# Optimization experiments

Hardware: AMD Instinct MI355X
Metric: run time of the kernel (lower is better)

Reference implementation:

```python
import jax, jax.numpy as jnp
import numpy as np

FILTERS = 512
DQK = FILTERS // 8  # 64


def setup_inputs() -> dict:
    key = jax.random.key(0)
    ks = jax.random.split(key, 7)
    B, H, W, C = 32, 32, 32, FILTERS
    x = jax.random.normal(ks[0], (B, H, W, C), dtype=jnp.float32)
    # 1x1 convs == per-pixel dense layers: weight [Cin, Cout], bias [Cout]
    def glorot(k, cin, cout):
        lim = np.sqrt(6.0 / (cin + cout)).astype(np.float32)
        return jax.random.uniform(k, (cin, cout), jnp.float32, -lim, lim)
    return {
        "x": x,
        "wq": glorot(ks[1], C, DQK), "bq": jnp.zeros((DQK,), jnp.float32),
        "wk": glorot(ks[2], C, DQK), "bk": jnp.zeros((DQK,), jnp.float32),
        "wv": glorot(ks[3], C, C),   "bv": jnp.zeros((C,), jnp.float32),
    }


def reference(x, wq, bq, wk, bk, wv, bv):
    B, H, W, C = x.shape
    N = H * W
    xf = x.reshape(B, N, C)                       # flatten spatial -> tokens
    q = xf @ wq + bq                              # [B, N, C//8]
    k = xf @ wk + bk                              # [B, N, C//8]
    v = xf @ wv + bv                              # [B, N, C]
    scale = 1.0 / jnp.sqrt(jnp.float32(C // 8))
    scores = jnp.einsum('bnd,bmd->bnm', q, k) * scale  # [B, N, N]
    probs = jax.nn.softmax(scores, axis=-1)
    attended = jnp.einsum('bnm,bmc->bnc', probs, v)    # [B, N, C]
    return attended.reshape(B, H, W, C) + x
```

## Files before the change

### kernel.cpp

```cpp
#include <hip/hip_runtime.h>
#include <stdint.h>

#define B_ 32
#define N_ 1024
#define C_ 512
#define D_ 64

typedef __attribute__((ext_vector_type(8))) __bf16 bf8;
typedef __attribute__((ext_vector_type(4))) float f32x4;

typedef const __attribute__((address_space(1))) void* gp_t;
typedef __attribute__((address_space(3))) void* lp_t;

__device__ inline void g2l16(const void* g, void* l) {
    __builtin_amdgcn_global_load_lds((gp_t)g, (lp_t)l, 16, 0, 0);
}

__device__ inline float b2f(unsigned short u) {
    return __uint_as_float(((unsigned)u) << 16);
}
__device__ inline unsigned short f2b(float f) {
    unsigned u = __float_as_uint(f);
    u += 0x7FFF + ((u >> 16) & 1);
    return (unsigned short)(u >> 16);
}

#define MFMA16(a, b, c) __builtin_amdgcn_mfma_f32_16x16x32_bf16((a), (b), (c), 0, 0, 0)

__device__ __forceinline__ void ld_frags(const unsigned short* As, const unsigned short* Bs,
                                         int wm, int wn, int lane,
                                         bf8 (&a)[2][4], bf8 (&bb)[2][4]) {
    #pragma unroll
    for (int kq = 0; kq < 2; ++kq) {
        #pragma unroll
        for (int ti = 0; ti < 4; ++ti)
            a[kq][ti] = *(const bf8*)&As[((wm * 4 + ti) * 2 + kq) * 512 + lane * 8];
        #pragma unroll
        for (int tj = 0; tj < 4; ++tj)
            bb[kq][tj] = *(const bf8*)&Bs[((wn * 4 + tj) * 2 + kq) * 512 + lane * 8];
    }
}

__device__ __forceinline__ void do_mfma(const bf8 (&a)[2][4], const bf8 (&bb)[2][4],
                                        f32x4 (&acc)[4][4]) {
    #pragma unroll
    for (int kq = 0; kq < 2; ++kq)
        #pragma unroll
        for (int ti = 0; ti < 4; ++ti)
            #pragma unroll
            for (int tj = 0; tj < 4; ++tj)
                acc[ti][tj] = MFMA16(a[kq][ti], bb[kq][tj], acc[ti][tj]);
}

__global__ __launch_bounds__(256) void prep(
    const float* __restrict__ x, unsigned short* __restrict__ xb,
    const float* __restrict__ wq, const float* __restrict__ wk,
    const float* __restrict__ wv, unsigned short* __restrict__ wt)
{
    int bid = blockIdx.x;
    if (bid < 16384) {
        int i = bid * 256 + threadIdx.x;
        float4 f = ((const float4*)x)[i];
        ushort4 o;
        o.x = f2b(f.x); o.y = f2b(f.y); o.z = f2b(f.z); o.w = f2b(f.w);
        ((ushort4*)xb)[i] = o;
    } else {
        int t = (bid - 16384) * 256 + threadIdx.x;
        int co = t >> 9;
        int ci = t & 511;
        const float* src;
        int col, cout;
        if (co < 64)       { src = wq; col = co;       cout = 64;  }
        else if (co < 128) { src = wk; col = co - 64;  cout = 64;  }
        else               { src = wv; col = co - 128; cout = 512; }
        wt[t] = f2b(src[(size_t)ci * cout + col]);
    }
}

__global__ __launch_bounds__(256) void qkv(
    const unsigned short* __restrict__ xb,
    const unsigned short* __restrict__ WT,
    const float* __restrict__ bq, const float* __restrict__ bk,
    const float* __restrict__ bv,
    unsigned short* __restrict__ q, unsigned short* __restrict__ k,
    unsigned short* __restrict__ vT)
{
    const int f_  = blockIdx.x;
    const int xcd = f_ & 7;
    const int s_  = f_ >> 3;
    const int rb  = xcd * 32 + s_ / 5;
    const int cb  = s_ % 5;

    const int tid = threadIdx.x;
    const int lane = tid & 63;
    const int wave = tid >> 6;
    const int wm = wave >> 1, wn = wave & 1;
    const int lr = lane & 15;
    const int lk = lane >> 4;

    __shared__ unsigned short SM[32768];
    unsigned short* TB = SM;

    const int row0 = rb * 128;
    const int col0 = cb * 128;

    f32x4 zero4 = {0.f, 0.f, 0.f, 0.f};
    f32x4 acc[4][4];
    #pragma unroll
    for (int i = 0; i < 4; ++i)
        #pragma unroll
        for (int j = 0; j < 4; ++j) acc[i][j] = zero4;

    auto stage = [&](int buf, int kk) {
        unsigned short* As = SM + buf * 8192;
        unsigned short* Bs = SM + 16384 + buf * 8192;
        #pragma unroll
        for (int i = 0; i < 4; ++i) {
            int f = wave * 4 + i;
            int t = f >> 1, kq = f & 1;
            g2l16(xb + (size_t)(row0 + t * 16 + lr) * C_ + kk + kq * 32 + lk * 8,
                  &As[f * 512]);
            g2l16(WT + (size_t)(col0 + t * 16 + lr) * C_ + kk + kq * 32 + lk * 8,
                  &Bs[f * 512]);
        }
    };

    stage(0, 0);
    stage(1, 64);
    int cur = 0;
    for (int t = 0; t < 6; ++t) {
        asm volatile("s_waitcnt vmcnt(8)" ::: "memory");
        __builtin_amdgcn_s_barrier();
        bf8 a[2][4], bb[2][4];
        ld_frags(SM + cur * 8192, SM + 16384 + cur * 8192, wm, wn, lane, a, bb);
        asm volatile("s_waitcnt lgkmcnt(0)" ::: "memory");
        __builtin_amdgcn_s_barrier();
        stage(cur, (t + 2) * 64);
        do_mfma(a, bb, acc);
        cur ^= 1;
    }
    {
        asm volatile("s_waitcnt vmcnt(8)" ::: "memory");
        __builtin_amdgcn_s_barrier();
        bf8 a[2][4], bb[2][4];
        ld_frags(SM + cur * 8192, SM + 16384 + cur * 8192, wm, wn, lane, a, bb);
        do_mfma(a, bb, acc);
        cur ^= 1;
    }
    {
        asm volatile("s_waitcnt vmcnt(0)" ::: "memory");
        __builtin_amdgcn_s_barrier();
        bf8 a[2][4], bb[2][4];
        ld_frags(SM + cur * 8192, SM + 16384 + cur * 8192, wm, wn, lane, a, bb);
        do_mfma(a, bb, acc);
    }

    if (cb == 0) {
        unsigned short* outp = (wn == 0) ? q : k;
        const float* bias = (wn == 0) ? bq : bk;
        #pragma unroll
        for (int ti = 0; ti < 4; ++ti)
            #pragma unroll
            for (int tj = 0; tj < 4; ++tj) {
                int col = tj * 16 + lr;
                float bi = bias[col];
                #pragma unroll
                for (int r = 0; r < 4; ++r) {
                    int row = row0 + wm * 64 + ti * 16 + lk * 4 + r;
                    outp[(size_t)row * D_ + col] = f2b(acc[ti][tj][r] + bi);
                }
            }
    } else {
        const int colv = (cb - 1) * 128;
        __syncthreads();
        #pragma unroll
        for (int ti = 0; ti < 4; ++ti)
            #pragma unroll
            for (int tj = 0; tj < 4; ++tj) {
                int c = wn * 64 + tj * 16 + lr;
                float bi = bv[colv + c];
                int tok = wm * 64 + ti * 16 + lk * 4;
                ushort4 o;
                o.x = f2b(acc[ti][tj][0] + bi);
                o.y = f2b(acc[ti][tj][1] + bi);
                o.z = f2b(acc[ti][tj][2] + bi);
                o.w = f2b(acc[ti][tj][3] + bi);
                *(ushort4*)&TB[c * 132 + tok] = o;
            }
        __syncthreads();
        const int b  = row0 >> 10;
        const int n0 = row0 & 1023;
        #pragma unroll
        for (int i = 0; i < 16; ++i) {
            int idx = tid + 256 * i;
            int c = idx >> 5, ch = idx & 31;
            ushort4 t4 = *(const ushort4*)&TB[c * 132 + ch * 4];
            *(ushort4*)&vT[((size_t)(b * C_ + colv + c)) * N_ + n0 + ch * 4] = t4;
        }
    }
}

#define SLD 1032
__global__ __launch_bounds__(256) void scores(
    const unsigned short* __restrict__ q,
    const unsigned short* __restrict__ k,
    unsigned short* __restrict__ P)
{
    const int f_  = blockIdx.x;
    const int xcd = f_ & 7;
    const int s_  = f_ >> 3;
    const int b   = xcd * 4 + (s_ >> 6);
    const int qt  = s_ & 63;

    const int tid = threadIdx.x, lane = tid & 63, wave = tid >> 6;
    const int lr = lane & 15, lk = lane >> 4;
    __shared__ unsigned short S[16 * SLD];

    const int n0 = qt * 16;
    const unsigned short* qrow = q + (size_t)(b * N_ + n0 + lr) * D_ + lk * 8;
    bf8 qa0 = *(const bf8*)(qrow);
    bf8 qa1 = *(const bf8*)(qrow + 32);

    const int m0w = wave * 256;
    #pragma unroll 4
    for (int mt = 0; mt < 16; ++mt) {
        int m = m0w + mt * 16;
        const unsigned short* krow = k + (size_t)(b * N_ + m + lr) * D_ + lk * 8;
        bf8 kb0 = *(const bf8*)(krow);
        bf8 kb1 = *(const bf8*)(krow + 32);
        f32x4 s = {0.f, 0.f, 0.f, 0.f};
        s = MFMA16(qa0, kb0, s);
        s = MFMA16(qa1, kb1, s);
        #pragma unroll
        for (int r = 0; r < 4; ++r)
            S[(lk * 4 + r) * SLD + m + lr] = f2b(s[r] * 0.125f);
    }
    __syncthreads();

    #pragma unroll
    for (int rr4 = 0; rr4 < 4; ++rr4) {
        int rr = wave * 4 + rr4;
        float vals[16];
        float mx = -1e30f;
        #pragma unroll
        for (int j = 0; j < 16; ++j) {
            vals[j] = b2f(S[rr * SLD + j * 64 + lane]);
            mx = fmaxf(mx, vals[j]);
        }
        #pragma unroll
        for (int off = 32; off; off >>= 1) mx = fmaxf(mx, __shfl_xor(mx, off));
        float sum = 0.f;
        #pragma unroll
        for (int j = 0; j < 16; ++j) { vals[j] = __expf(vals[j] - mx); sum += vals[j]; }
        #pragma unroll
        for (int off = 32; off; off >>= 1) sum += __shfl_xor(sum, off);
        float inv = 1.f / sum;
        unsigned short* pp = P + (size_t)(b * N_ + n0 + rr) * N_;
        #pragma unroll
        for (int j = 0; j < 16; ++j) pp[j * 64 + lane] = f2b(vals[j] * inv);
    }
}

__global__ __launch_bounds__(512, 4) void pv(
    const unsigned short* __restrict__ P,
    const unsigned short* __restrict__ vT,
    const float* __restrict__ x,
    float* __restrict__ out)
{
    const int f_   = blockIdx.x;
    const int xcd  = f_ & 7;
    const int s_   = f_ >> 3;
    const int b    = xcd * 4 + (s_ >> 4);
    const int w_   = s_ & 15;
    const int m0   = (w_ & 3) * 256;
    const int c0   = (w_ >> 2) * 128;

    const int tid = threadIdx.x, lane = tid & 63, wave = tid >> 6;
    const int wm = wave >> 1;
    const int wn = wave & 1;
    const int lr = lane & 15, lk = lane >> 4;

    __shared__ unsigned short SM[36864];

    f32x4 zero4 = {0.f, 0.f, 0.f, 0.f};
    f32x4 acc[4][4];
    #pragma unroll
    for (int i = 0; i < 4; ++i)
        #pragma unroll
        for (int j = 0; j < 4; ++j) acc[i][j] = zero4;

    const unsigned short* Pb = P  + (size_t)b * N_ * N_;
    const unsigned short* Vb = vT + (size_t)b * C_ * N_;

    auto stage = [&](int t32, int buf) {
        unsigned short* Ab = SM + buf * 12288;
        unsigned short* Bb = Ab + 8192;
        const int kk = t32 * 32;
        #pragma unroll
        for (int i = 0; i < 3; ++i) {
            int f = wave * 3 + i;
            if (f < 16) {
                g2l16(Pb + (size_t)(m0 + f * 16 + lr) * N_ + kk + lk * 8,
                      &Ab[f * 512]);
            } else {
                int g = f - 16;
                g2l16(Vb + (size_t)(c0 + g * 16 + lr) * N_ + kk + lk * 8,
                      &Bb[g * 512]);
            }
        }
    };

    auto compute = [&](int buf) {
        const unsigned short* Ab = SM + buf * 12288;
        const unsigned short* Bb = Ab + 8192;
        bf8 a[4], bb[4];
        #pragma unroll
        for (int ti = 0; ti < 4; ++ti)
            a[ti] = *(const bf8*)&Ab[(wm * 4 + ti) * 512 + lane * 8];
        #pragma unroll
        for (int tj = 0; tj < 4; ++tj)
            bb[tj] = *(const bf8*)&Bb[(wn * 4 + tj) * 512 + lane * 8];
        asm volatile("s_waitcnt lgkmcnt(0)" ::: "memory");
        __builtin_amdgcn_sched_barrier(0);
        __builtin_amdgcn_s_setprio(1);
        #pragma unroll
        for (int ti = 0; ti < 4; ++ti)
            #pragma unroll
            for (int tj = 0; tj < 4; ++tj)
                acc[ti][tj] = MFMA16(a[ti], bb[tj], acc[ti][tj]);
        __builtin_amdgcn_s_setprio(0);
    };

    stage(0, 0); stage(1, 1);
    int bufc = 0;
    for (int t = 0; t < 30; ++t) {
        asm volatile("s_waitcnt vmcnt(3)" ::: "memory");
        __builtin_amdgcn_s_barrier();
        int bufs = bufc + 2; if (bufs >= 3) bufs -= 3;
        stage(t + 2, bufs);
        compute(bufc);
        bufc = bufc + 1; if (bufc >= 3) bufc -= 3;
    }
    {
        asm volatile("s_waitcnt vmcnt(3)" ::: "memory");
        __builtin_amdgcn_s_barrier();
        compute(bufc);
        bufc = bufc + 1; if (bufc >= 3) bufc -= 3;
    }
    {
        asm volatile("s_waitcnt vmcnt(0)" ::: "memory");
        __builtin_amdgcn_s_barrier();
        compute(bufc);
    }

    #pragma unroll
    for (int ti = 0; ti < 4; ++ti)
        #pragma unroll
        for (int tj = 0; tj < 4; ++tj) {
            int col = c0 + wn * 64 + tj * 16 + lr;
            #pragma unroll
            for (int r = 0; r < 4; ++r) {
                int row = m0 + wm * 64 + ti * 16 + lk * 4 + r;
                size_t idx = (size_t)(b * N_ + row) * C_ + col;
                out[idx] = acc[ti][tj][r] + x[idx];
            }
        }
}

extern "C" void kernel_launch(void* const* d_in, const int* in_sizes, int n_in,
                              void* d_out, int out_size, void* d_ws, size_t ws_size,
                              hipStream_t stream) {
    (void)in_sizes; (void)n_in; (void)out_size; (void)ws_size;
    const float* xf = (const float*)d_in[0];
    const float* wq = (const float*)d_in[1];
    const float* bq = (const float*)d_in[2];
    const float* wk = (const float*)d_in[3];
    const float* bk = (const float*)d_in[4];
    const float* wv = (const float*)d_in[5];
    const float* bv = (const float*)d_in[6];
    float* out = (float*)d_out;

    char* ws = (char*)d_ws;
    unsigned short* qb  = (unsigned short*)(ws);
    unsigned short* kb  = (unsigned short*)(ws + 4194304);
    unsigned short* vTb = (unsigned short*)(ws + 8388608);
    unsigned short* WT  = (unsigned short*)(ws + 41943040);
    unsigned short* xb  = (unsigned short*)(ws + 42598400);
    unsigned short* Pb  = (unsigned short*)(ws + 41943040);

    prep<<<17664, 256, 0, stream>>>(xf, xb, wq, wk, wv, WT);
    qkv<<<1280, 256, 0, stream>>>(xb, WT, bq, bk, bv, qb, kb, vTb);
    scores<<<2048, 256, 0, stream>>>(qb, kb, Pb);
    pv<<<512, 512, 0, stream>>>(Pb, vTb, xf, out);
}
```

Measured before the change: 265.6 us.

## Restructure QKV GEMM into 512-thread blocks with triple-buffered K=32 pipeline

```diff
diff --git a/kernel.cpp b/kernel.cpp
--- a/kernel.cpp
+++ b/kernel.cpp
@@ -26,31 +26,6 @@
 }
 
 #define MFMA16(a, b, c) __builtin_amdgcn_mfma_f32_16x16x32_bf16((a), (b), (c), 0, 0, 0)
-
-__device__ __forceinline__ void ld_frags(const unsigned short* As, const unsigned short* Bs,
-                                         int wm, int wn, int lane,
-                                         bf8 (&a)[2][4], bf8 (&bb)[2][4]) {
-    #pragma unroll
-    for (int kq = 0; kq < 2; ++kq) {
-        #pragma unroll
-        for (int ti = 0; ti < 4; ++ti)
-            a[kq][ti] = *(const bf8*)&As[((wm * 4 + ti) * 2 + kq) * 512 + lane * 8];
-        #pragma unroll
-        for (int tj = 0; tj < 4; ++tj)
-            bb[kq][tj] = *(const bf8*)&Bs[((wn * 4 + tj) * 2 + kq) * 512 + lane * 8];
-    }
-}
-
-__device__ __forceinline__ void do_mfma(const bf8 (&a)[2][4], const bf8 (&bb)[2][4],
-                                        f32x4 (&acc)[4][4]) {
-    #pragma unroll
-    for (int kq = 0; kq < 2; ++kq)
-        #pragma unroll
-        for (int ti = 0; ti < 4; ++ti)
-            #pragma unroll
-            for (int tj = 0; tj < 4; ++tj)
-                acc[ti][tj] = MFMA16(a[kq][ti], bb[kq][tj], acc[ti][tj]);
-}
 
 __global__ __launch_bounds__(256) void prep(
     const float* __restrict__ x, unsigned short* __restrict__ xb,
@@ -77,7 +52,7 @@
     }
 }
 
-__global__ __launch_bounds__(256) void qkv(
+__global__ __launch_bounds__(512, 4) void qkv(
     const unsigned short* __restrict__ xb,
     const unsigned short* __restrict__ WT,
     const float* __restrict__ bq, const float* __restrict__ bk,
@@ -88,21 +63,30 @@
     const int f_  = blockIdx.x;
     const int xcd = f_ & 7;
     const int s_  = f_ >> 3;
-    const int rb  = xcd * 32 + s_ / 5;
-    const int cb  = s_ % 5;
-
-    const int tid = threadIdx.x;
-    const int lane = tid & 63;
-    const int wave = tid >> 6;
-    const int wm = wave >> 1, wn = wave & 1;
-    const int lr = lane & 15;
-    const int lk = lane >> 4;
-
-    __shared__ unsigned short SM[32768];
-    unsigned short* TB = SM;
-
-    const int row0 = rb * 128;
-    const int col0 = cb * 128;
+    const bool isv = (s_ < 64);
+
+    int row0, wcol0, nA, wm, wn;
+    const int tid = threadIdx.x, lane = tid & 63, wave = tid >> 6;
+    int cbv = 0, rbv = 0;
+    if (isv) {
+        rbv   = xcd * 32 + (s_ >> 1);
+        cbv   = s_ & 1;
+        row0  = rbv * 128;
+        wcol0 = 128 + cbv * 256;
+        nA    = 8;
+        wm    = wave >> 2;
+        wn    = wave & 3;
+    } else {
+        int rbq = xcd * 16 + (s_ - 64);
+        row0  = rbq * 256;
+        wcol0 = 0;
+        nA    = 16;
+        wm    = wave >> 1;
+        wn    = wave & 1;
+    }
+    const int lr = lane & 15, lk = lane >> 4;
+
+    __shared__ unsigned short SM[36864];
 
     f32x4 zero4 = {0.f, 0.f, 0.f, 0.f};
     f32x4 acc[4][4];
@@ -111,51 +95,86 @@
         #pragma unroll
         for (int j = 0; j < 4; ++j) acc[i][j] = zero4;
 
-    auto stage = [&](int buf, int kk) {
-        unsigned short* As = SM + buf * 8192;
-        unsigned short* Bs = SM + 16384 + buf * 8192;
-        #pragma unroll
-        for (int i = 0; i < 4; ++i) {
-            int f = wave * 4 + i;
-            int t = f >> 1, kq = f & 1;
-            g2l16(xb + (size_t)(row0 + t * 16 + lr) * C_ + kk + kq * 32 + lk * 8,
-                  &As[f * 512]);
-            g2l16(WT + (size_t)(col0 + t * 16 + lr) * C_ + kk + kq * 32 + lk * 8,
-                  &Bs[f * 512]);
+    auto stage = [&](int t32, int buf) {
+        unsigned short* Ab = SM + buf * 12288;
+        unsigned short* Bb = Ab + nA * 512;
+        const int kk = t32 * 32;
+        #pragma unroll
+        for (int i = 0; i < 3; ++i) {
+            int f = wave * 3 + i;
+            if (f < nA) {
+                g2l16(xb + (size_t)(row0 + f * 16 + lr) * C_ + kk + lk * 8,
+                      &Ab[f * 512]);
+            } else {
+                int g = f - nA;
+                g2l16(WT + (size_t)(wcol0 + g * 16 + lr) * C_ + kk + lk * 8,
+                      &Bb[g * 512]);
+            }
         }
     };
 
-    stage(0, 0);
-    stage(1, 64);
-    int cur = 0;
-    for (int t = 0; t < 6; ++t) {
-        asm volatile("s_waitcnt vmcnt(8)" ::: "memory");
-        __builtin_amdgcn_s_barrier();
-        bf8 a[2][4], bb[2][4];
-        ld_frags(SM + cur * 8192, SM + 16384 + cur * 8192, wm, wn, lane, a, bb);
+    auto compute = [&](int buf) {
+        const unsigned short* Ab = SM + buf * 12288;
+        const unsigned short* Bb = Ab + nA * 512;
+        bf8 a[4], bb[4];
+        #pragma unroll
+        for (int ti = 0; ti < 4; ++ti)
+            a[ti] = *(const bf8*)&Ab[(wm * 4 + ti) * 512 + lane * 8];
+        #pragma unroll
+        for (int tj = 0; tj < 4; ++tj)
+            bb[tj] = *(const bf8*)&Bb[(wn * 4 + tj) * 512 + lane * 8];
         asm volatile("s_waitcnt lgkmcnt(0)" ::: "memory");
-        __builtin_amdgcn_s_barrier();
-        stage(cur, (t + 2) * 64);
-        do_mfma(a, bb, acc);
-        cur ^= 1;
+        __builtin_amdgcn_sched_barrier(0);
+        __builtin_amdgcn_s_setprio(1);
+        #pragma unroll
+        for (int ti = 0; ti < 4; ++ti)
+            #pragma unroll
+            for (int tj = 0; tj < 4; ++tj)
+                acc[ti][tj] = MFMA16(a[ti], bb[tj], acc[ti][tj]);
+        __builtin_amdgcn_s_setprio(0);
+    };
+
+    stage(0, 0); stage(1, 1);
+    int bufc = 0;
+    for (int t = 0; t < 14; ++t) {
+        asm volatile("s_waitcnt vmcnt(3)" ::: "memory");
+        __builtin_amdgcn_s_barrier();
+        int bufs = bufc + 2; if (bufs >= 3) bufs -= 3;
+        stage(t + 2, bufs);
+        compute(bufc);
+        bufc = bufc + 1; if (bufc >= 3) bufc -= 3;
     }
     {
-        asm volatile("s_waitcnt vmcnt(8)" ::: "memory");
-        __builtin_amdgcn_s_barrier();
-        bf8 a[2][4], bb[2][4];
-        ld_frags(SM + cur * 8192, SM + 16384 + cur * 8192, wm, wn, lane, a, bb);
-        do_mfma(a, bb, acc);
-        cur ^= 1;
+        asm volatile("s_waitcnt vmcnt(3)" ::: "memory");
+        __builtin_amdgcn_s_barrier();
+        compute(bufc);
+        bufc = bufc + 1; if (bufc >= 3) bufc -= 3;
     }
     {
         asm volatile("s_waitcnt vmcnt(0)" ::: "memory");
         __builtin_amdgcn_s_barrier();
-        bf8 a[2][4], bb[2][4];
-        ld_frags(SM + cur * 8192, SM + 16384 + cur * 8192, wm, wn, lane, a, bb);
-        do_mfma(a, bb, acc);
-    }
-
-    if (cb == 0) {
+        compute(bufc);
+    }
+
+    if (isv) {
+        const int b  = rbv >> 3;
+        const int n0 = (rbv & 7) * 128;
+        #pragma unroll
+        for (int tj = 0; tj < 4; ++tj) {
+            int col = cbv * 256 + wn * 64 + tj * 16 + lr;
+            float bi = bv[col];
+            #pragma unroll
+            for (int ti = 0; ti < 4; ++ti) {
+                int nb = n0 + wm * 64 + ti * 16 + lk * 4;
+                ushort4 o;
+                o.x = f2b(acc[ti][tj][0] + bi);
+                o.y = f2b(acc[ti][tj][1] + bi);
+                o.z = f2b(acc[ti][tj][2] + bi);
+                o.w = f2b(acc[ti][tj][3] + bi);
+                *(ushort4*)&vT[((size_t)(b * C_ + col)) * N_ + nb] = o;
+            }
+        }
+    } else {
         unsigned short* outp = (wn == 0) ? q : k;
         const float* bias = (wn == 0) ? bq : bk;
         #pragma unroll
@@ -170,33 +189,6 @@
                     outp[(size_t)row * D_ + col] = f2b(acc[ti][tj][r] + bi);
                 }
             }
-    } else {
-        const int colv = (cb - 1) * 128;
-        __syncthreads();
-        #pragma unroll
-        for (int ti = 0; ti < 4; ++ti)
-            #pragma unroll
-            for (int tj = 0; tj < 4; ++tj) {
-                int c = wn * 64 + tj * 16 + lr;
-                float bi = bv[colv + c];
-                int tok = wm * 64 + ti * 16 + lk * 4;
-                ushort4 o;
-                o.x = f2b(acc[ti][tj][0] + bi);
-                o.y = f2b(acc[ti][tj][1] + bi);
-                o.z = f2b(acc[ti][tj][2] + bi);
-                o.w = f2b(acc[ti][tj][3] + bi);
-                *(ushort4*)&TB[c * 132 + tok] = o;
-            }
-        __syncthreads();
-        const int b  = row0 >> 10;
-        const int n0 = row0 & 1023;
-        #pragma unroll
-        for (int i = 0; i < 16; ++i) {
-            int idx = tid + 256 * i;
-            int c = idx >> 5, ch = idx & 31;
-            ushort4 t4 = *(const ushort4*)&TB[c * 132 + ch * 4];
-            *(ushort4*)&vT[((size_t)(b * C_ + colv + c)) * N_ + n0 + ch * 4] = t4;
-        }
     }
 }
 
@@ -389,7 +381,7 @@
     unsigned short* Pb  = (unsigned short*)(ws + 41943040);
 
     prep<<<17664, 256, 0, stream>>>(xf, xb, wq, wk, wv, WT);
-    qkv<<<1280, 256, 0, stream>>>(xb, WT, bq, bk, bv, qb, kb, vTb);
+    qkv<<<640, 512, 0, stream>>>(xb, WT, bq, bk, bv, qb, kb, vTb);
     scores<<<2048, 256, 0, stream>>>(qb, kb, Pb);
     pv<<<512, 512, 0, stream>>>(Pb, vTb, xf, out);
 }
```

After: 269.3 us. No clear change (+1.4%).
